# Performance work log

Hardware: AMD Instinct MI355X
Metric: run time of the kernel (lower is better)

Reference implementation:

```python
import jax, jax.numpy as jnp
import numpy as np

B, N, IN_F = 16, 1024, 256
HEADS, OUT_F = 4, 64
NEG_SLOPE = 0.2
CLAMP_MIN = -1e9
MASK_VAL = -9e15


def setup_inputs() -> dict:
    key = jax.random.key(0)
    k1, k2, k3, k4 = jax.random.split(key, 4)
    x = jax.random.normal(k1, (B, N, IN_F), dtype=jnp.float32)
    adj = jax.random.randint(k2, (B, N, N), 0, 2, dtype=jnp.int32)
    # Linear weight, stored as (in, heads*out) so y = x @ W (xavier-uniform scale)
    lim_w = float(np.sqrt(6.0 / (IN_F + HEADS * OUT_F)))
    W = jax.random.uniform(k3, (IN_F, HEADS * OUT_F), dtype=jnp.float32,
                           minval=-lim_w, maxval=lim_w)
    lim_a = float(np.sqrt(6.0 / (2 * OUT_F + HEADS)))
    a = jax.random.uniform(k4, (2 * OUT_F, HEADS), dtype=jnp.float32,
                           minval=-lim_a, maxval=lim_a)
    return {"x": x, "adj": adj, "W": W, "a": a}


def reference(x, adj, W, a):
    Bs, Ns, _ = x.shape
    # Projection: (B,N,H,D)
    h = (x @ W).reshape(Bs, Ns, HEADS, OUT_F)
    # cat([h_i, h_j]) . a == h_i . a_src + h_j . a_dst  (exact same math, no O(N^2*2D) tensor)
    a_src, a_dst = a[:OUT_F], a[OUT_F:]          # each (D, H)
    s_src = jnp.einsum('bnhd,dh->bnh', h, a_src)  # score contribution of node i
    s_dst = jnp.einsum('bnhd,dh->bnh', h, a_dst)  # score contribution of node j
    e = jax.nn.leaky_relu(s_src[:, :, None, :] + s_dst[:, None, :, :],
                          negative_slope=NEG_SLOPE)  # (B,N,N,H)
    # match original: subtract unmasked row max, clamp, then mask, then softmax over j
    e = e - jnp.max(e, axis=2, keepdims=True)
    e = jnp.maximum(e, CLAMP_MIN)
    att = jnp.where(adj[..., None] > 0, e, MASK_VAL)
    att = jax.nn.softmax(att, axis=2)
    h_prime = jnp.einsum('bijh,bjhd->bihd', att, h)  # (B,N,H,D)
    return h_prime.reshape(Bs, Ns, HEADS * OUT_F)
```

## Files before the change

kernel.cpp:

```cpp
#include <hip/hip_runtime.h>
#include <hip/hip_bf16.h>

#define B_   16
#define N_   1024
#define INF_ 256
#define NH_  4
#define HD_  256
#define L2E  1.4426950408889634f

typedef __attribute__((ext_vector_type(8))) short short8;
typedef __attribute__((ext_vector_type(4))) float f32x4;

__device__ __forceinline__ float bf2f(unsigned short u) {
    union { unsigned int i; float f; } v; v.i = ((unsigned int)u) << 16; return v.f;
}
__device__ __forceinline__ unsigned short f2bf(float f) {
    union { float f; unsigned int i; } v; v.f = f;
    unsigned int x = v.i;
    return (unsigned short)((x + 0x7fffu + ((x >> 16) & 1u)) >> 16);
}
__device__ __forceinline__ unsigned int cvt_pk_bf16(float lo, float hi) {
    unsigned int r;
    asm("v_cvt_pk_bf16_f32 %0, %1, %2" : "=v"(r) : "v"(lo), "v"(hi));
    return r;
}

__global__ __launch_bounds__(256) void k_prep(const int* __restrict__ adj,
                                              const float* __restrict__ W,
                                              unsigned int* __restrict__ pb,
                                              unsigned short* __restrict__ wswz)
{
    int bx = blockIdx.x, t = threadIdx.x;
    if (bx < 2048) {
        int wave = t >> 6, lane = t & 63;
        int row = bx * 8 + wave * 2 + (lane >> 5);
        int w   = lane & 31;
        const int4* ar = (const int4*)(adj + ((long)row << 10) + w * 32);
        unsigned int u = 0;
        #pragma unroll
        for (int k = 0; k < 8; k++) {
            int4 a = ar[k];
            u |= ((unsigned)a.x) << (4 * k);
            u |= ((unsigned)a.y) << (4 * k + 1);
            u |= ((unsigned)a.z) << (4 * k + 2);
            u |= ((unsigned)a.w) << (4 * k + 3);
        }
        pb[((long)row << 5) + w] = u;
    } else {
        int slot = (bx - 2048) * 256 + t;
        int kstep = slot >> 10;
        int nt    = (slot >> 6) & 15;
        int lane  = slot & 63;
        int k0 = kstep * 32 + (lane >> 4) * 8;
        int n  = nt * 16 + (lane & 15);
        ushort4 o0, o1;
        o0.x = f2bf(W[(k0 + 0) * HD_ + n]);
        o0.y = f2bf(W[(k0 + 1) * HD_ + n]);
        o0.z = f2bf(W[(k0 + 2) * HD_ + n]);
        o0.w = f2bf(W[(k0 + 3) * HD_ + n]);
        o1.x = f2bf(W[(k0 + 4) * HD_ + n]);
        o1.y = f2bf(W[(k0 + 5) * HD_ + n]);
        o1.z = f2bf(W[(k0 + 6) * HD_ + n]);
        o1.w = f2bf(W[(k0 + 7) * HD_ + n]);
        *(ushort4*)&wswz[(long)slot * 8]     = o0;
        *(ushort4*)&wswz[(long)slot * 8 + 4] = o1;
    }
}

__global__ __launch_bounds__(256) void k_gemm_h(
    const float* __restrict__ x, const float* __restrict__ a,
    const unsigned short* __restrict__ wswz,
    unsigned short* __restrict__ hswz,
    float* __restrict__ esr, float2* __restrict__ edst)
{
    __shared__ unsigned short xls[16][264];
    int t = threadIdx.x;
    int blk = blockIdx.x;
    int row0 = blk * 16;
    int b  = blk >> 6;
    int n0 = row0 & 1023;

    {
        int sr = t >> 4, sc = (t & 15) * 16;
        const float* xp = x + (long)(row0 + sr) * INF_ + sc;
        float4 v0 = ((const float4*)xp)[0];
        float4 v1 = ((const float4*)xp)[1];
        float4 v2 = ((const float4*)xp)[2];
        float4 v3 = ((const float4*)xp)[3];
        ushort4 u0 = {f2bf(v0.x), f2bf(v0.y), f2bf(v0.z), f2bf(v0.w)};
        ushort4 u1 = {f2bf(v1.x), f2bf(v1.y), f2bf(v1.z), f2bf(v1.w)};
        ushort4 u2 = {f2bf(v2.x), f2bf(v2.y), f2bf(v2.z), f2bf(v2.w)};
        ushort4 u3 = {f2bf(v3.x), f2bf(v3.y), f2bf(v3.z), f2bf(v3.w)};
        *(ushort4*)&xls[sr][sc]      = u0;
        *(ushort4*)&xls[sr][sc + 4]  = u1;
        *(ushort4*)&xls[sr][sc + 8]  = u2;
        *(ushort4*)&xls[sr][sc + 12] = u3;
    }
    __syncthreads();

    int wave = t >> 6, lane = t & 63, quad = lane >> 4, l15 = lane & 15;
    f32x4 acc[4];
    #pragma unroll
    for (int i = 0; i < 4; i++) acc[i] = (f32x4){0.f, 0.f, 0.f, 0.f};

    #pragma unroll
    for (int ks = 0; ks < 8; ks++) {
        short8 af = *(const short8*)&xls[l15][ks * 32 + quad * 8];
        #pragma unroll
        for (int nt = 0; nt < 4; nt++) {
            short8 bf = *(const short8*)(wswz +
                ((long)((ks * 16 + wave * 4 + nt) * 64 + lane)) * 8);
            acc[nt] = __builtin_amdgcn_mfma_f32_16x16x32_bf16(af, bf, acc[nt], 0, 0, 0);
        }
    }

    int q0 = (quad & 1) * 4;
    int qd = ((row0 & 31) + quad * 4) >> 3;
    long bj32 = row0 >> 5;
    #pragma unroll
    for (int nt = 0; nt < 4; nt++) {
        int dg = wave * 4 + nt;
        long idx8 = (bj32 * 16 + dg) * 64 + qd * 16 + l15;
        ushort4 o = {f2bf(acc[nt][0]), f2bf(acc[nt][1]),
                     f2bf(acc[nt][2]), f2bf(acc[nt][3])};
        *(ushort4*)&hswz[idx8 * 8 + q0] = o;
    }

    float as_[4], ad_[4];
    #pragma unroll
    for (int nt = 0; nt < 4; nt++) {
        int d = nt * 16 + l15;
        as_[nt] = a[d * NH_ + wave];
        ad_[nt] = a[(64 + d) * NH_ + wave];
    }
    #pragma unroll
    for (int r = 0; r < 4; r++) {
        float ps = acc[0][r] * as_[0] + acc[1][r] * as_[1]
                 + acc[2][r] * as_[2] + acc[3][r] * as_[3];
        float pd = acc[0][r] * ad_[0] + acc[1][r] * ad_[1]
                 + acc[2][r] * ad_[2] + acc[3][r] * ad_[3];
        #pragma unroll
        for (int m = 1; m < 16; m <<= 1) {
            ps += __shfl_xor(ps, m);
            pd += __shfl_xor(pd, m);
        }
        if (l15 == 0) {
            int row = n0 + quad * 4 + r;
            float s1 = ps * L2E, s2 = pd * L2E;
            esr[((long)b * NH_ + wave) * N_ + row] = __builtin_exp2f(-0.8f * s1);
            edst[((long)b * NH_ + wave) * N_ + row] =
                make_float2(__builtin_exp2f(s2), __builtin_exp2f(0.2f * s2));
        }
    }
}

__global__ __launch_bounds__(512, 8) void k_attn(
    const unsigned int* __restrict__ pb, const unsigned short* __restrict__ hswz,
    const float* __restrict__ esr, const float2* __restrict__ edst,
    float* __restrict__ out)
{
    __shared__ uint2 mtab[16];
    __shared__ float accb[4][64][20];

    int t = threadIdx.x;
    int b  = blockIdx.x >> 6, ig = blockIdx.x & 63;
    int i0 = ig * 16;
    int wave = t >> 6, lane = t & 63, quad = lane >> 4, l15 = lane & 15;
    int hh = wave & 3, jh = wave >> 2;

    if (t < 16) {
        int k = t;
        unsigned int w0 = ((k & 1) ? 0xffffu : 0u) | ((k & 2) ? 0xffff0000u : 0u);
        unsigned int w1 = ((k & 4) ? 0xffffu : 0u) | ((k & 8) ? 0xffff0000u : 0u);
        mtab[k] = make_uint2(w0, w1);
    }
    __syncthreads();

    float r0 = esr[((long)(b * NH_ + hh)) * N_ + i0 + l15];
    const float2* edp = edst + ((long)(b * NH_ + hh)) * N_ + jh * 512;
    long grow0 = ((long)b << 10) + i0 + l15;
    const unsigned int* pb0 = pb + (grow0 << 5) + jh * 16;

    f32x4 acc[4], dn;
    #pragma unroll
    for (int i = 0; i < 4; i++) acc[i] = (f32x4){0.f, 0.f, 0.f, 0.f};
    dn = (f32x4){0.f, 0.f, 0.f, 0.f};
    short8 ones;
    #pragma unroll
    for (int i = 0; i < 8; i++) ones[i] = (short)0x3F80;

    int shq = quad * 8;

    #pragma unroll 4
    for (int jc = 0; jc < 16; jc++) {
        unsigned int m0 = (pb0[jc] >> shq) & 0xffu;
        const float4* ej = (const float4*)(edp + jc * 32 + quad * 8);

        union { unsigned int u[4]; short8 s; } p0;
        #pragma unroll
        for (int qp = 0; qp < 4; qp++) {
            float4 d = ej[qp];
            float lo = fmaxf(d.x, r0 * d.y);
            float hi = fmaxf(d.z, r0 * d.w);
            p0.u[qp] = cvt_pk_bf16(lo, hi);
        }
        uint2 ma = mtab[m0 & 15u], mb = mtab[m0 >> 4];
        p0.u[0] &= ma.x; p0.u[1] &= ma.y; p0.u[2] &= mb.x; p0.u[3] &= mb.y;

        long s8 = ((long)(b * 32 + jh * 16 + jc)) * 1024;
        #pragma unroll
        for (int idt = 0; idt < 4; idt++) {
            short8 bf = *(const short8*)(hswz + (s8 + (hh * 4 + idt) * 64 + lane) * 8);
            acc[idt] = __builtin_amdgcn_mfma_f32_16x16x32_bf16(p0.s, bf, acc[idt], 0, 0, 0);
        }
        dn = __builtin_amdgcn_mfma_f32_16x16x32_bf16(p0.s, ones, dn, 0, 0, 0);
    }

    if (jh == 1) {
        #pragma unroll
        for (int idt = 0; idt < 4; idt++)
            *(f32x4*)&accb[hh][lane][idt * 4] = acc[idt];
        *(f32x4*)&accb[hh][lane][16] = dn;
    }
    __syncthreads();

    if (jh == 0) {
        f32x4 od = *(const f32x4*)&accb[hh][lane][16];
        float inv[4];
        #pragma unroll
        for (int r = 0; r < 4; r++) inv[r] = 1.0f / (dn[r] + od[r]);
        #pragma unroll
        for (int idt = 0; idt < 4; idt++) {
            f32x4 o = *(const f32x4*)&accb[hh][lane][idt * 4];
            int col = hh * 64 + idt * 16 + l15;
            #pragma unroll
            for (int r = 0; r < 4; r++) {
                long row_g = (long)b * N_ + i0 + quad * 4 + r;
                out[row_g * HD_ + col] = (acc[idt][r] + o[r]) * inv[r];
            }
        }
    }
}

extern "C" void kernel_launch(void* const* d_in, const int* in_sizes, int n_in,
                              void* d_out, int out_size, void* d_ws, size_t ws_size,
                              hipStream_t stream) {
    const float* x   = (const float*)d_in[0];
    const int*   adj = (const int*)d_in[1];
    const float* W   = (const float*)d_in[2];
    const float* a   = (const float*)d_in[3];
    float* out = (float*)d_out;

    unsigned int* pb      = (unsigned int*)d_ws;
    unsigned short* hswz  = (unsigned short*)(pb + 524288);
    unsigned short* wswz  = hswz + (long)B_ * N_ * HD_;
    float* esr   = (float*)(wswz + INF_ * HD_);
    float2* edst = (float2*)(esr + (long)B_ * NH_ * N_);

    k_prep<<<2080, 256, 0, stream>>>(adj, W, pb, wswz);
    k_gemm_h<<<1024, 256, 0, stream>>>(x, a, wswz, hswz, esr, edst);
    k_attn<<<1024, 512, 0, stream>>>(pb, hswz, esr, edst, out);
}
```

Measured before the change: 165.7 us.

## Process 32 query rows per block with 16 waves and swizzled block order

The attention kernel now handles 32 query rows per block instead of 16. Each wave reuses its loaded h tiles and edst values across two row tiles, and the j dimension is split four ways across 1024-thread blocks. Block indices are swizzled to spread consecutive blocks across batches, and partial sums are reduced in two LDS rounds. This cuts global loads of h and edst per output, at the cost of more registers, extra barriers, and half as many blocks.

```diff
diff --git a/kernel.cpp b/kernel.cpp
--- a/kernel.cpp
+++ b/kernel.cpp
@@ -154,17 +154,19 @@
     }
 }
 
-__global__ __launch_bounds__(512, 8) void k_attn(
+__global__ __launch_bounds__(1024, 8) void k_attn(
     const unsigned int* __restrict__ pb, const unsigned short* __restrict__ hswz,
     const float* __restrict__ esr, const float2* __restrict__ edst,
     float* __restrict__ out)
 {
     __shared__ uint2 mtab[16];
-    __shared__ float accb[4][64][20];
+    __shared__ float accb[3][4][64][20];
 
     int t = threadIdx.x;
-    int b  = blockIdx.x >> 6, ig = blockIdx.x & 63;
-    int i0 = ig * 16;
+    int bid = blockIdx.x;
+    int swz = (bid & 7) * 64 + (bid >> 3);
+    int b  = swz >> 5, ig = swz & 31;
+    int i0 = ig * 32;
     int wave = t >> 6, lane = t & 63, quad = lane >> 4, l15 = lane & 15;
     int hh = wave & 3, jh = wave >> 2;
 
@@ -177,66 +179,101 @@
     __syncthreads();
 
     float r0 = esr[((long)(b * NH_ + hh)) * N_ + i0 + l15];
-    const float2* edp = edst + ((long)(b * NH_ + hh)) * N_ + jh * 512;
+    float r1 = esr[((long)(b * NH_ + hh)) * N_ + i0 + 16 + l15];
+    const float2* edp = edst + ((long)(b * NH_ + hh)) * N_ + jh * 256;
     long grow0 = ((long)b << 10) + i0 + l15;
-    const unsigned int* pb0 = pb + (grow0 << 5) + jh * 16;
-
-    f32x4 acc[4], dn;
-    #pragma unroll
-    for (int i = 0; i < 4; i++) acc[i] = (f32x4){0.f, 0.f, 0.f, 0.f};
-    dn = (f32x4){0.f, 0.f, 0.f, 0.f};
+    const unsigned int* pb0 = pb + (grow0 << 5) + jh * 8;
+    const unsigned int* pb1 = pb0 + (16 << 5);
+
+    f32x4 acc0[4], acc1[4], dn0, dn1;
+    #pragma unroll
+    for (int i = 0; i < 4; i++) {
+        acc0[i] = (f32x4){0.f, 0.f, 0.f, 0.f};
+        acc1[i] = (f32x4){0.f, 0.f, 0.f, 0.f};
+    }
+    dn0 = (f32x4){0.f, 0.f, 0.f, 0.f};
+    dn1 = (f32x4){0.f, 0.f, 0.f, 0.f};
     short8 ones;
     #pragma unroll
     for (int i = 0; i < 8; i++) ones[i] = (short)0x3F80;
 
     int shq = quad * 8;
 
-    #pragma unroll 4
-    for (int jc = 0; jc < 16; jc++) {
+    #pragma unroll 2
+    for (int jc = 0; jc < 8; jc++) {
         unsigned int m0 = (pb0[jc] >> shq) & 0xffu;
+        unsigned int m1 = (pb1[jc] >> shq) & 0xffu;
         const float4* ej = (const float4*)(edp + jc * 32 + quad * 8);
 
-        union { unsigned int u[4]; short8 s; } p0;
+        union { unsigned int u[4]; short8 s; } p0, p1;
         #pragma unroll
         for (int qp = 0; qp < 4; qp++) {
             float4 d = ej[qp];
-            float lo = fmaxf(d.x, r0 * d.y);
-            float hi = fmaxf(d.z, r0 * d.w);
-            p0.u[qp] = cvt_pk_bf16(lo, hi);
-        }
-        uint2 ma = mtab[m0 & 15u], mb = mtab[m0 >> 4];
-        p0.u[0] &= ma.x; p0.u[1] &= ma.y; p0.u[2] &= mb.x; p0.u[3] &= mb.y;
-
-        long s8 = ((long)(b * 32 + jh * 16 + jc)) * 1024;
+            p0.u[qp] = cvt_pk_bf16(fmaxf(d.x, r0 * d.y), fmaxf(d.z, r0 * d.w));
+            p1.u[qp] = cvt_pk_bf16(fmaxf(d.x, r1 * d.y), fmaxf(d.z, r1 * d.w));
+        }
+        uint2 ma0 = mtab[m0 & 15u], mb0 = mtab[m0 >> 4];
+        uint2 ma1 = mtab[m1 & 15u], mb1 = mtab[m1 >> 4];
+        p0.u[0] &= ma0.x; p0.u[1] &= ma0.y; p0.u[2] &= mb0.x; p0.u[3] &= mb0.y;
+        p1.u[0] &= ma1.x; p1.u[1] &= ma1.y; p1.u[2] &= mb1.x; p1.u[3] &= mb1.y;
+
+        long s8 = ((long)(b * 32 + jh * 8 + jc)) * 1024;
         #pragma unroll
         for (int idt = 0; idt < 4; idt++) {
             short8 bf = *(const short8*)(hswz + (s8 + (hh * 4 + idt) * 64 + lane) * 8);
-            acc[idt] = __builtin_amdgcn_mfma_f32_16x16x32_bf16(p0.s, bf, acc[idt], 0, 0, 0);
-        }
-        dn = __builtin_amdgcn_mfma_f32_16x16x32_bf16(p0.s, ones, dn, 0, 0, 0);
-    }
-
-    if (jh == 1) {
+            acc0[idt] = __builtin_amdgcn_mfma_f32_16x16x32_bf16(p0.s, bf, acc0[idt], 0, 0, 0);
+            acc1[idt] = __builtin_amdgcn_mfma_f32_16x16x32_bf16(p1.s, bf, acc1[idt], 0, 0, 0);
+        }
+        dn0 = __builtin_amdgcn_mfma_f32_16x16x32_bf16(p0.s, ones, dn0, 0, 0, 0);
+        dn1 = __builtin_amdgcn_mfma_f32_16x16x32_bf16(p1.s, ones, dn1, 0, 0, 0);
+    }
+
+    if (jh) {
         #pragma unroll
         for (int idt = 0; idt < 4; idt++)
-            *(f32x4*)&accb[hh][lane][idt * 4] = acc[idt];
-        *(f32x4*)&accb[hh][lane][16] = dn;
-    }
-    __syncthreads();
-
-    if (jh == 0) {
-        f32x4 od = *(const f32x4*)&accb[hh][lane][16];
-        float inv[4];
-        #pragma unroll
-        for (int r = 0; r < 4; r++) inv[r] = 1.0f / (dn[r] + od[r]);
+            *(f32x4*)&accb[jh - 1][hh][lane][idt * 4] = acc0[idt];
+        *(f32x4*)&accb[jh - 1][hh][lane][16] = dn0;
+    }
+    __syncthreads();
+    if (!jh) {
+        #pragma unroll
+        for (int s = 0; s < 3; s++) {
+            #pragma unroll
+            for (int idt = 0; idt < 4; idt++)
+                acc0[idt] += *(const f32x4*)&accb[s][hh][lane][idt * 4];
+            dn0 += *(const f32x4*)&accb[s][hh][lane][16];
+        }
+    }
+    __syncthreads();
+    if (jh) {
+        #pragma unroll
+        for (int idt = 0; idt < 4; idt++)
+            *(f32x4*)&accb[jh - 1][hh][lane][idt * 4] = acc1[idt];
+        *(f32x4*)&accb[jh - 1][hh][lane][16] = dn1;
+    }
+    __syncthreads();
+    if (!jh) {
+        #pragma unroll
+        for (int s = 0; s < 3; s++) {
+            #pragma unroll
+            for (int idt = 0; idt < 4; idt++)
+                acc1[idt] += *(const f32x4*)&accb[s][hh][lane][idt * 4];
+            dn1 += *(const f32x4*)&accb[s][hh][lane][16];
+        }
+        float inv0[4], inv1[4];
+        #pragma unroll
+        for (int r = 0; r < 4; r++) {
+            inv0[r] = 1.0f / dn0[r];
+            inv1[r] = 1.0f / dn1[r];
+        }
         #pragma unroll
         for (int idt = 0; idt < 4; idt++) {
-            f32x4 o = *(const f32x4*)&accb[hh][lane][idt * 4];
             int col = hh * 64 + idt * 16 + l15;
             #pragma unroll
             for (int r = 0; r < 4; r++) {
                 long row_g = (long)b * N_ + i0 + quad * 4 + r;
-                out[row_g * HD_ + col] = (acc[idt][r] + o[r]) * inv[r];
+                out[row_g * HD_ + col] = acc0[idt][r] * inv0[r];
+                out[(row_g + 16) * HD_ + col] = acc1[idt][r] * inv1[r];
             }
         }
     }
@@ -259,5 +296,5 @@
 
     k_prep<<<2080, 256, 0, stream>>>(adj, W, pb, wswz);
     k_gemm_h<<<1024, 256, 0, stream>>>(x, a, wswz, hswz, esr, edst);
-    k_attn<<<1024, 512, 0, stream>>>(pb, hswz, esr, edst, out);
-}
+    k_attn<<<512, 1024, 0, stream>>>(pb, hswz, esr, edst, out);
+}
```

Result: slower. 211.5 us (+27.7%).

## Stage h tiles into LDS with double-buffered async loads in attention kernel

Applied to the files above, without the earlier changes.

The attention kernel now covers 32 query rows per block instead of 16, with the two wave groups splitting rows rather than the j range. This removes the cross-wave LDS reduction, and each h tile is shared by twice as many rows. h tiles are copied into double-buffered LDS with global_load_lds so the next tile loads while the current one is consumed by MFMA. Block IDs are swizzled to group blocks of the same batch. In exchange there are two barriers per j-chunk, half as many blocks, and a lower occupancy hint.

```diff
diff --git a/kernel.cpp b/kernel.cpp
--- a/kernel.cpp
+++ b/kernel.cpp
@@ -23,6 +23,11 @@
     unsigned int r;
     asm("v_cvt_pk_bf16_f32 %0, %1, %2" : "=v"(r) : "v"(lo), "v"(hi));
     return r;
+}
+__device__ __forceinline__ void glds16(const void* g, void* l) {
+    __builtin_amdgcn_global_load_lds(
+        (const __attribute__((address_space(1))) unsigned int*)g,
+        (__attribute__((address_space(3))) unsigned int*)l, 16, 0, 0);
 }
 
 __global__ __launch_bounds__(256) void k_prep(const int* __restrict__ adj,
@@ -154,19 +159,22 @@
     }
 }
 
-__global__ __launch_bounds__(512, 8) void k_attn(
+__global__ __launch_bounds__(512, 4) void k_attn(
     const unsigned int* __restrict__ pb, const unsigned short* __restrict__ hswz,
     const float* __restrict__ esr, const float2* __restrict__ edst,
     float* __restrict__ out)
 {
     __shared__ uint2 mtab[16];
-    __shared__ float accb[4][64][20];
+    __shared__ unsigned short hbuf0[8192];
+    __shared__ unsigned short hbuf1[8192];
 
     int t = threadIdx.x;
-    int b  = blockIdx.x >> 6, ig = blockIdx.x & 63;
-    int i0 = ig * 16;
+    int bid = blockIdx.x;
+    int swz = (bid & 7) * 64 + (bid >> 3);
+    int b  = swz >> 5, ig = swz & 31;
+    int i0 = ig * 32;
     int wave = t >> 6, lane = t & 63, quad = lane >> 4, l15 = lane & 15;
-    int hh = wave & 3, jh = wave >> 2;
+    int hh = wave & 3, sw = wave >> 2;
 
     if (t < 16) {
         int k = t;
@@ -174,12 +182,12 @@
         unsigned int w1 = ((k & 4) ? 0xffffu : 0u) | ((k & 8) ? 0xffff0000u : 0u);
         mtab[k] = make_uint2(w0, w1);
     }
-    __syncthreads();
-
-    float r0 = esr[((long)(b * NH_ + hh)) * N_ + i0 + l15];
-    const float2* edp = edst + ((long)(b * NH_ + hh)) * N_ + jh * 512;
-    long grow0 = ((long)b << 10) + i0 + l15;
-    const unsigned int* pb0 = pb + (grow0 << 5) + jh * 16;
+
+    int irow = i0 + sw * 16 + l15;
+    float r0 = esr[((long)(b * NH_ + hh)) * N_ + irow];
+    const float2* edp = edst + ((long)(b * NH_ + hh)) * N_;
+    const unsigned int* pbrow = pb + ((((long)b << 10) + irow) << 5);
+    const unsigned short* hsrc = hswz + (((long)b * 32) << 13);
 
     f32x4 acc[4], dn;
     #pragma unroll
@@ -191,53 +199,51 @@
 
     int shq = quad * 8;
 
-    #pragma unroll 4
-    for (int jc = 0; jc < 16; jc++) {
-        unsigned int m0 = (pb0[jc] >> shq) & 0xffu;
-        const float4* ej = (const float4*)(edp + jc * 32 + quad * 8);
-
-        union { unsigned int u[4]; short8 s; } p0;
-        #pragma unroll
-        for (int qp = 0; qp < 4; qp++) {
-            float4 d = ej[qp];
-            float lo = fmaxf(d.x, r0 * d.y);
-            float hi = fmaxf(d.z, r0 * d.w);
-            p0.u[qp] = cvt_pk_bf16(lo, hi);
-        }
-        uint2 ma = mtab[m0 & 15u], mb = mtab[m0 >> 4];
-        p0.u[0] &= ma.x; p0.u[1] &= ma.y; p0.u[2] &= mb.x; p0.u[3] &= mb.y;
-
-        long s8 = ((long)(b * 32 + jh * 16 + jc)) * 1024;
-        #pragma unroll
-        for (int idt = 0; idt < 4; idt++) {
-            short8 bf = *(const short8*)(hswz + (s8 + (hh * 4 + idt) * 64 + lane) * 8);
-            acc[idt] = __builtin_amdgcn_mfma_f32_16x16x32_bf16(p0.s, bf, acc[idt], 0, 0, 0);
-        }
-        dn = __builtin_amdgcn_mfma_f32_16x16x32_bf16(p0.s, ones, dn, 0, 0, 0);
-    }
-
-    if (jh == 1) {
-        #pragma unroll
-        for (int idt = 0; idt < 4; idt++)
-            *(f32x4*)&accb[hh][lane][idt * 4] = acc[idt];
-        *(f32x4*)&accb[hh][lane][16] = dn;
-    }
-    __syncthreads();
-
-    if (jh == 0) {
-        f32x4 od = *(const f32x4*)&accb[hh][lane][16];
-        float inv[4];
-        #pragma unroll
-        for (int r = 0; r < 4; r++) inv[r] = 1.0f / (dn[r] + od[r]);
-        #pragma unroll
-        for (int idt = 0; idt < 4; idt++) {
-            f32x4 o = *(const f32x4*)&accb[hh][lane][idt * 4];
-            int col = hh * 64 + idt * 16 + l15;
-            #pragma unroll
-            for (int r = 0; r < 4; r++) {
-                long row_g = (long)b * N_ + i0 + quad * 4 + r;
-                out[row_g * HD_ + col] = (acc[idt][r] + o[r]) * inv[r];
-            }
+    #define STAGE(BUF, JC) { \
+        const unsigned short* g = hsrc + (((long)(JC)) << 13); \
+        glds16(g + (wave * 128 + lane) * 8,      &BUF[wave * 1024]); \
+        glds16(g + (wave * 128 + 64 + lane) * 8, &BUF[wave * 1024 + 512]); }
+
+    #define COMPUTE(JC, BUF) { \
+        unsigned int m0 = (pbrow[(JC)] >> shq) & 0xffu; \
+        const float4* ej = (const float4*)(edp + (JC) * 32 + quad * 8); \
+        union { unsigned int u[4]; short8 s; } p0; \
+        _Pragma("unroll") \
+        for (int qp = 0; qp < 4; qp++) { \
+            float4 d = ej[qp]; \
+            p0.u[qp] = cvt_pk_bf16(fmaxf(d.x, r0 * d.y), fmaxf(d.z, r0 * d.w)); \
+        } \
+        uint2 ma = mtab[m0 & 15u], mb = mtab[m0 >> 4]; \
+        p0.u[0] &= ma.x; p0.u[1] &= ma.y; p0.u[2] &= mb.x; p0.u[3] &= mb.y; \
+        _Pragma("unroll") \
+        for (int idt = 0; idt < 4; idt++) { \
+            short8 bf = *(const short8*)&BUF[(hh * 4 + idt) * 512 + lane * 8]; \
+            acc[idt] = __builtin_amdgcn_mfma_f32_16x16x32_bf16(p0.s, bf, acc[idt], 0, 0, 0); \
+        } \
+        dn = __builtin_amdgcn_mfma_f32_16x16x32_bf16(p0.s, ones, dn, 0, 0, 0); }
+
+    STAGE(hbuf0, 0);
+    for (int jc = 0; jc < 32; jc += 2) {
+        __syncthreads();
+        STAGE(hbuf1, jc + 1);
+        COMPUTE(jc, hbuf0);
+        __syncthreads();
+        if (jc + 2 < 32) STAGE(hbuf0, jc + 2);
+        COMPUTE(jc + 1, hbuf1);
+    }
+    #undef STAGE
+    #undef COMPUTE
+
+    float inv[4];
+    #pragma unroll
+    for (int r = 0; r < 4; r++) inv[r] = 1.0f / dn[r];
+    #pragma unroll
+    for (int idt = 0; idt < 4; idt++) {
+        int col = hh * 64 + idt * 16 + l15;
+        #pragma unroll
+        for (int r = 0; r < 4; r++) {
+            long row_g = (long)b * N_ + i0 + sw * 16 + quad * 4 + r;
+            out[row_g * HD_ + col] = acc[idt][r] * inv[r];
         }
     }
 }
@@ -259,5 +265,5 @@
 
     k_prep<<<2080, 256, 0, stream>>>(adj, W, pb, wswz);
     k_gemm_h<<<1024, 256, 0, stream>>>(x, a, wswz, hswz, esr, edst);
-    k_attn<<<1024, 512, 0, stream>>>(pb, hswz, esr, edst, out);
-}
+    k_attn<<<512, 512, 0, stream>>>(pb, hswz, esr, edst, out);
+}
```

Measured after the change: 167.4 us. Within noise of the previous version (+1.0%).

## Restructure attention blocks per (batch, head, row-group) with LDS-staged edst and transposed adjacency bits

Applied to the files above, without the earlier changes.

The attention kernel now gives each 1024-thread block one batch/head and 256 query rows, with each wave handling 16 rows across all 1024 keys. This removes the split-j partial reduction through shared memory and its extra barrier. The per-head edst vector is staged once into LDS instead of being read from global per wave. Packed adjacency bits are stored transposed so consecutive rows are coalesced, and block IDs are swizzled for locality. The trade-off is fewer, larger blocks (256), which may hurt occupancy and load balance, and a longer serial loop per wave.

```diff
diff --git a/kernel.cpp b/kernel.cpp
--- a/kernel.cpp
+++ b/kernel.cpp
@@ -45,7 +45,7 @@
             u |= ((unsigned)a.z) << (4 * k + 2);
             u |= ((unsigned)a.w) << (4 * k + 3);
         }
-        pb[((long)row << 5) + w] = u;
+        pb[((long)w << 14) + row] = u;
     } else {
         int slot = (bx - 2048) * 256 + t;
         int kstep = slot >> 10;
@@ -154,20 +154,25 @@
     }
 }
 
-__global__ __launch_bounds__(512, 8) void k_attn(
+__global__ __launch_bounds__(1024, 4) void k_attn(
     const unsigned int* __restrict__ pb, const unsigned short* __restrict__ hswz,
     const float* __restrict__ esr, const float2* __restrict__ edst,
     float* __restrict__ out)
 {
+    __shared__ float2 esb[1024];
     __shared__ uint2 mtab[16];
-    __shared__ float accb[4][64][20];
 
     int t = threadIdx.x;
-    int b  = blockIdx.x >> 6, ig = blockIdx.x & 63;
-    int i0 = ig * 16;
+    int bid = blockIdx.x;
+    int swz = (bid & 7) * 32 + (bid >> 3);
+    int b  = swz >> 4;
+    int hh = (swz >> 2) & 3;
+    int rg = swz & 3;
+    int row0 = rg * 256;
+
     int wave = t >> 6, lane = t & 63, quad = lane >> 4, l15 = lane & 15;
-    int hh = wave & 3, jh = wave >> 2;
-
+
+    esb[t] = edst[((long)(b * NH_ + hh)) * N_ + t];
     if (t < 16) {
         int k = t;
         unsigned int w0 = ((k & 1) ? 0xffffu : 0u) | ((k & 2) ? 0xffff0000u : 0u);
@@ -176,10 +181,9 @@
     }
     __syncthreads();
 
-    float r0 = esr[((long)(b * NH_ + hh)) * N_ + i0 + l15];
-    const float2* edp = edst + ((long)(b * NH_ + hh)) * N_ + jh * 512;
-    long grow0 = ((long)b << 10) + i0 + l15;
-    const unsigned int* pb0 = pb + (grow0 << 5) + jh * 16;
+    int irow = row0 + wave * 16 + l15;
+    float r0 = esr[((long)(b * NH_ + hh)) * N_ + irow];
+    const unsigned int* pbw = pb + ((long)b << 10) + irow;
 
     f32x4 acc[4], dn;
     #pragma unroll
@@ -192,22 +196,20 @@
     int shq = quad * 8;
 
     #pragma unroll 4
-    for (int jc = 0; jc < 16; jc++) {
-        unsigned int m0 = (pb0[jc] >> shq) & 0xffu;
-        const float4* ej = (const float4*)(edp + jc * 32 + quad * 8);
+    for (int jc = 0; jc < 32; jc++) {
+        unsigned int m0 = (pbw[((long)jc << 14)] >> shq) & 0xffu;
+        const f32x4* ej = (const f32x4*)&esb[jc * 32 + quad * 8];
 
         union { unsigned int u[4]; short8 s; } p0;
         #pragma unroll
         for (int qp = 0; qp < 4; qp++) {
-            float4 d = ej[qp];
-            float lo = fmaxf(d.x, r0 * d.y);
-            float hi = fmaxf(d.z, r0 * d.w);
-            p0.u[qp] = cvt_pk_bf16(lo, hi);
+            f32x4 d = ej[qp];
+            p0.u[qp] = cvt_pk_bf16(fmaxf(d[0], r0 * d[1]), fmaxf(d[2], r0 * d[3]));
         }
         uint2 ma = mtab[m0 & 15u], mb = mtab[m0 >> 4];
         p0.u[0] &= ma.x; p0.u[1] &= ma.y; p0.u[2] &= mb.x; p0.u[3] &= mb.y;
 
-        long s8 = ((long)(b * 32 + jh * 16 + jc)) * 1024;
+        long s8 = ((long)(b * 32 + jc)) * 1024;
         #pragma unroll
         for (int idt = 0; idt < 4; idt++) {
             short8 bf = *(const short8*)(hswz + (s8 + (hh * 4 + idt) * 64 + lane) * 8);
@@ -216,28 +218,16 @@
         dn = __builtin_amdgcn_mfma_f32_16x16x32_bf16(p0.s, ones, dn, 0, 0, 0);
     }
 
-    if (jh == 1) {
-        #pragma unroll
-        for (int idt = 0; idt < 4; idt++)
-            *(f32x4*)&accb[hh][lane][idt * 4] = acc[idt];
-        *(f32x4*)&accb[hh][lane][16] = dn;
-    }
-    __syncthreads();
-
-    if (jh == 0) {
-        f32x4 od = *(const f32x4*)&accb[hh][lane][16];
-        float inv[4];
-        #pragma unroll
-        for (int r = 0; r < 4; r++) inv[r] = 1.0f / (dn[r] + od[r]);
-        #pragma unroll
-        for (int idt = 0; idt < 4; idt++) {
-            f32x4 o = *(const f32x4*)&accb[hh][lane][idt * 4];
-            int col = hh * 64 + idt * 16 + l15;
-            #pragma unroll
-            for (int r = 0; r < 4; r++) {
-                long row_g = (long)b * N_ + i0 + quad * 4 + r;
-                out[row_g * HD_ + col] = (acc[idt][r] + o[r]) * inv[r];
-            }
+    float inv[4];
+    #pragma unroll
+    for (int r = 0; r < 4; r++) inv[r] = 1.0f / dn[r];
+    #pragma unroll
+    for (int idt = 0; idt < 4; idt++) {
+        int col = hh * 64 + idt * 16 + l15;
+        #pragma unroll
+        for (int r = 0; r < 4; r++) {
+            long row_g = (long)b * N_ + row0 + wave * 16 + quad * 4 + r;
+            out[row_g * HD_ + col] = acc[idt][r] * inv[r];
         }
     }
 }
@@ -259,5 +249,5 @@
 
     k_prep<<<2080, 256, 0, stream>>>(adj, W, pb, wswz);
     k_gemm_h<<<1024, 256, 0, stream>>>(x, a, wswz, hswz, esr, edst);
-    k_attn<<<1024, 512, 0, stream>>>(pb, hswz, esr, edst, out);
-}
+    k_attn<<<256, 1024, 0, stream>>>(pb, hswz, esr, edst, out);
+}
```

Measured after the change: 149.5 us. 9.8% less time.
